# Optimization experiments

Hardware: AMD Instinct MI355X
Metric: run time of the kernel (lower is better)

## Reference

```python
import jax, jax.numpy as jnp
import numpy as np

D_MIN, D_MAX, D_COUNT = 2.0, 22.0, 36  # RFdiffusion rbf() constants


def _rbf(D):
    # D: [..., L, L] -> [..., L, L, D_COUNT]
    mu = jnp.linspace(D_MIN, D_MAX, D_COUNT, dtype=D.dtype)
    sigma = (D_MAX - D_MIN) / D_COUNT
    return jnp.exp(-(((D[..., None] - mu) / sigma) ** 2))


def _layernorm(x, w, b, eps=1e-5):
    mu = jnp.mean(x, axis=-1, keepdims=True)
    var = jnp.var(x, axis=-1, keepdims=True)
    return (x - mu) * jax.lax.rsqrt(var + eps) * w + b


def setup_inputs() -> dict:
    key = jax.random.key(0)
    ks = jax.random.split(key, 8)
    B, L, d_state, d_pair, h, d_rbf = 1, 512, 256, 128, 32, D_COUNT
    s = lambda d: 1.0 / np.sqrt(d)
    return {
        "xyz": jax.random.normal(ks[0], (B, L, 3, 3), jnp.float32) * 5.0,
        "state": jax.random.normal(ks[1], (B, L, d_state), jnp.float32),
        "ln_w": jnp.ones((d_state,), jnp.float32),
        "ln_b": jnp.zeros((d_state,), jnp.float32),
        "w_rbf": jax.random.normal(ks[2], (d_rbf, d_pair), jnp.float32) * s(d_rbf),
        "b_rbf": jnp.zeros((d_pair,), jnp.float32),
        "w_left": jax.random.normal(ks[3], (d_state, h), jnp.float32) * s(d_state),
        "b_left": jnp.zeros((h,), jnp.float32),
        "w_right": jax.random.normal(ks[4], (d_state, h), jnp.float32) * s(d_state),
        "b_right": jnp.zeros((h,), jnp.float32),
        "w_gate": jax.random.normal(ks[5], (h * h, d_pair), jnp.float32) * s(h * h),
        "b_gate": jnp.zeros((d_pair,), jnp.float32),
    }


def reference(xyz, state, ln_w, ln_b, w_rbf, b_rbf, w_left, b_left,
              w_right, b_right, w_gate, b_gate):
    B, L = xyz.shape[:2]
    h = w_left.shape[1]
    d_pair = w_rbf.shape[1]

    # pairwise CA distances -> RBF features -> project to pair dim
    cas = xyz[:, :, 1]                                        # [B, L, 3]
    d2 = jnp.sum((cas[:, :, None, :] - cas[:, None, :, :]) ** 2, axis=-1)
    dist = jnp.sqrt(jnp.maximum(d2, 1e-12))                   # [B, L, L]
    rbf_feat = _rbf(dist) @ w_rbf + b_rbf                     # [B, L, L, d_pair]

    # gated pair bias: sigmoid(to_gate(outer(left, right)))
    st = _layernorm(state, ln_w, ln_b)
    left = st @ w_left + b_left                               # [B, L, h]
    right = st @ w_right + b_right                            # [B, L, h]

    # Algebraically identical to einsum('bli,bmj->blmij') -> reshape -> Linear,
    # but factored through the projection weight to avoid the O(L^2 h^2) tensor.
    Wg = w_gate.reshape(h, h, d_pair)                         # flatten order i*h+j
    t = jnp.einsum('bli,ijp->bljp', left, Wg)                 # [B, L, h, d_pair]
    logits = jnp.einsum('bljp,bmj->blmp', t, right) + b_gate  # [B, L, L, d_pair]
    gate = jax.nn.sigmoid(logits)

    return gate * rbf_feat
```

## Files before the change

kernel.cpp:

```cpp
#include <hip/hip_runtime.h>
#include <hip/hip_fp16.h>

typedef _Float16 half8 __attribute__((ext_vector_type(8)));
typedef float floatx4 __attribute__((ext_vector_type(4)));

#define LSEQ 512
#define DSTATE 256
#define DPAIR 128
#define HH 32
#define DRBF 36

#define MUSTEP (20.0f / 35.0f)
#define INVSIG 1.8f

__global__ __launch_bounds__(256) void prologA(
    const float* __restrict__ state, const float* __restrict__ ln_w,
    const float* __restrict__ ln_b, const float* __restrict__ w_left,
    const float* __restrict__ b_left, const float* __restrict__ w_right,
    const float* __restrict__ b_right, float* __restrict__ left,
    _Float16* __restrict__ right_h) {
  __shared__ float stS[DSTATE];
  __shared__ float redS[4], redQ[4];
  __shared__ float part[4][64];
  const int l = blockIdx.x, tid = threadIdx.x;

  float x = state[l * DSTATE + tid];
  float s = x, q = x * x;
  #pragma unroll
  for (int o = 32; o > 0; o >>= 1) {
    s += __shfl_down(s, o);
    q += __shfl_down(q, o);
  }
  if ((tid & 63) == 0) { redS[tid >> 6] = s; redQ[tid >> 6] = q; }
  __syncthreads();
  float tot = redS[0] + redS[1] + redS[2] + redS[3];
  float totq = redQ[0] + redQ[1] + redQ[2] + redQ[3];
  float mean = tot * (1.0f / DSTATE);
  float var = totq * (1.0f / DSTATE) - mean * mean;
  float inv = rsqrtf(var + 1e-5f);
  stS[tid] = (x - mean) * inv * ln_w[tid] + ln_b[tid];
  __syncthreads();

  const int j = tid & 63;
  const int quarter = tid >> 6;
  const float* __restrict__ w = (j < HH) ? (w_left + j) : (w_right + (j - HH));
  const int c0 = quarter * 64;
  float acc = 0.0f;
  #pragma unroll 8
  for (int cc = 0; cc < 64; ++cc) acc += stS[c0 + cc] * w[(c0 + cc) * HH];
  part[quarter][j] = acc;
  __syncthreads();
  if (tid < 64) {
    float sum = part[0][tid] + part[1][tid] + part[2][tid] + part[3][tid];
    if (tid < HH)
      left[l * HH + tid] = sum + b_left[tid];
    else
      right_h[l * HH + (tid - HH)] = (_Float16)(sum + b_right[tid - HH]);
  }
}

__global__ __launch_bounds__(256) void prologB(
    const float* __restrict__ w_gate, const float* __restrict__ w_rbf,
    const float* __restrict__ left, _Float16* __restrict__ tT,
    _Float16* __restrict__ w_rbfT) {
  const int tid = threadIdx.x;
  if (blockIdx.x == 1024) {
    for (int e = tid; e < DPAIR * 64; e += 256) {
      int p = e >> 6, k = e & 63;
      w_rbfT[e] = (k < DRBF) ? (_Float16)w_rbf[k * DPAIR + p] : (_Float16)0.0f;
    }
    return;
  }
  const int c = blockIdx.x & 15;
  const int lc = blockIdx.x >> 4;
  const int j = tid & 31;
  const int p = c * 8 + (tid >> 5);

  float wcol[32];
  #pragma unroll
  for (int i = 0; i < 32; ++i) wcol[i] = w_gate[(i * HH + j) * DPAIR + p];

  const int l0 = lc * 8;
  #pragma unroll
  for (int l = l0; l < l0 + 8; ++l) {
    const float* __restrict__ lf = left + l * HH;
    float acc = 0.0f;
    #pragma unroll
    for (int i = 0; i < 32; ++i) acc += lf[i] * wcol[i];
    tT[l * (DPAIR * HH) + c * 256 + tid] = (_Float16)acc;
  }
}

__global__ __launch_bounds__(256) void mainC(
    const float* __restrict__ xyz, const float* __restrict__ b_rbf,
    const float* __restrict__ b_gate, const _Float16* __restrict__ right_h,
    const _Float16* __restrict__ tT, const _Float16* __restrict__ w_rbfT,
    float* __restrict__ out) {
  __shared__ _Float16 sT[DPAIR * HH];
  __shared__ _Float16 sW[DPAIR * 64];
  const int l = blockIdx.x >> 1;
  const int half = blockIdx.x & 1;
  const int tid = threadIdx.x;
  const int wave = tid >> 6;
  const int lane = tid & 63;
  const int ln16 = lane & 15;
  const int quad = lane >> 4;

  {
    const uint4* __restrict__ src = (const uint4*)(tT + (size_t)l * (DPAIR * HH));
    uint4* dst = (uint4*)sT;
    #pragma unroll
    for (int i = 0; i < 2; ++i) dst[tid + 256 * i] = src[tid + 256 * i];
    const uint4* __restrict__ src2 = (const uint4*)w_rbfT;
    uint4* dst2 = (uint4*)sW;
    #pragma unroll
    for (int i = 0; i < 4; ++i) dst2[tid + 256 * i] = src2[tid + 256 * i];
  }

  const float clx = xyz[l * 9 + 3];
  const float cly = xyz[l * 9 + 4];
  const float clz = xyz[l * 9 + 5];

  float bg[8], br[8];
  #pragma unroll
  for (int pt = 0; pt < 8; ++pt) {
    bg[pt] = b_gate[pt * 16 + ln16];
    br[pt] = b_rbf[pt * 16 + ln16];
  }

  __syncthreads();

  const int mt0 = half * 16;
  for (int mt = mt0 + wave; mt < mt0 + 16; mt += 4) {
    const int mA = mt * 16 + ln16;
    half8 Ar = *(const half8*)(right_h + mA * HH + quad * 8);

    const float dx = clx - xyz[mA * 9 + 3];
    const float dy = cly - xyz[mA * 9 + 4];
    const float dz = clz - xyz[mA * 9 + 5];
    const float d = sqrtf(fmaxf(dx * dx + dy * dy + dz * dz, 1e-12f));

    half8 A0, A1;
    #pragma unroll
    for (int jj = 0; jj < 8; ++jj) {
      const int k = quad * 8 + jj;
      const float u = (d - (2.0f + (float)k * MUSTEP)) * INVSIG;
      A0[jj] = (_Float16)__expf(-u * u);
    }
    #pragma unroll
    for (int jj = 0; jj < 8; ++jj) {
      const int k = 32 + quad * 8 + jj;
      float v = 0.0f;
      if (k < DRBF) {
        const float u = (d - (2.0f + (float)k * MUSTEP)) * INVSIG;
        v = __expf(-u * u);
      }
      A1[jj] = (_Float16)v;
    }

    #pragma unroll
    for (int pt = 0; pt < 8; ++pt) {
      const int p = pt * 16 + ln16;
      half8 Bt = *(const half8*)(sT + p * HH + quad * 8);
      half8 Bw0 = *(const half8*)(sW + p * 64 + quad * 8);
      half8 Bw1 = *(const half8*)(sW + p * 64 + 32 + quad * 8);

      floatx4 accL = {0.f, 0.f, 0.f, 0.f};
      floatx4 accR = {0.f, 0.f, 0.f, 0.f};
      accL = __builtin_amdgcn_mfma_f32_16x16x32_f16(Ar, Bt, accL, 0, 0, 0);
      accR = __builtin_amdgcn_mfma_f32_16x16x32_f16(A0, Bw0, accR, 0, 0, 0);
      accR = __builtin_amdgcn_mfma_f32_16x16x32_f16(A1, Bw1, accR, 0, 0, 0);

      float* orow = out + ((size_t)l * LSEQ + mt * 16 + quad * 4) * DPAIR + p;
      #pragma unroll
      for (int i = 0; i < 4; ++i) {
        const float logit = accL[i] + bg[pt];
        const float gate = __builtin_amdgcn_rcpf(1.0f + __expf(-logit));
        const float feat = accR[i] + br[pt];
        orow[i * DPAIR] = gate * feat;
      }
    }
  }
}

extern "C" void kernel_launch(void* const* d_in, const int* in_sizes, int n_in,
                              void* d_out, int out_size, void* d_ws,
                              size_t ws_size, hipStream_t stream) {
  const float* xyz = (const float*)d_in[0];
  const float* state = (const float*)d_in[1];
  const float* ln_w = (const float*)d_in[2];
  const float* ln_b = (const float*)d_in[3];
  const float* w_rbf = (const float*)d_in[4];
  const float* b_rbf = (const float*)d_in[5];
  const float* w_left = (const float*)d_in[6];
  const float* b_left = (const float*)d_in[7];
  const float* w_right = (const float*)d_in[8];
  const float* b_right = (const float*)d_in[9];
  const float* w_gate = (const float*)d_in[10];
  const float* b_gate = (const float*)d_in[11];
  float* out = (float*)d_out;

  char* ws = (char*)d_ws;
  float* left = (float*)ws;
  _Float16* right_h = (_Float16*)(ws + 65536);
  _Float16* tT = (_Float16*)(ws + 98304);
  _Float16* w_rbfT = (_Float16*)(ws + 4292608);

  prologA<<<512, 256, 0, stream>>>(state, ln_w, ln_b, w_left, b_left, w_right,
                                   b_right, left, right_h);
  prologB<<<1025, 256, 0, stream>>>(w_gate, w_rbf, left, tT, w_rbfT);
  mainC<<<1024, 256, 0, stream>>>(xyz, b_rbf, b_gate, right_h, tT, w_rbfT, out);
}
```

Before: 190.2 us.

## Fuse layernorm/projection and gate-weight contraction into one prolog kernel

```diff
diff --git a/kernel.cpp b/kernel.cpp
--- a/kernel.cpp
+++ b/kernel.cpp
@@ -13,81 +13,124 @@
 #define MUSTEP (20.0f / 35.0f)
 #define INVSIG 1.8f
 
-__global__ __launch_bounds__(256) void prologA(
+__global__ __launch_bounds__(256) void prolog(
     const float* __restrict__ state, const float* __restrict__ ln_w,
     const float* __restrict__ ln_b, const float* __restrict__ w_left,
     const float* __restrict__ b_left, const float* __restrict__ w_right,
-    const float* __restrict__ b_right, float* __restrict__ left,
-    _Float16* __restrict__ right_h) {
-  __shared__ float stS[DSTATE];
-  __shared__ float redS[4], redQ[4];
-  __shared__ float part[4][64];
-  const int l = blockIdx.x, tid = threadIdx.x;
-
-  float x = state[l * DSTATE + tid];
-  float s = x, q = x * x;
-  #pragma unroll
-  for (int o = 32; o > 0; o >>= 1) {
-    s += __shfl_down(s, o);
-    q += __shfl_down(q, o);
-  }
-  if ((tid & 63) == 0) { redS[tid >> 6] = s; redQ[tid >> 6] = q; }
-  __syncthreads();
-  float tot = redS[0] + redS[1] + redS[2] + redS[3];
-  float totq = redQ[0] + redQ[1] + redQ[2] + redQ[3];
-  float mean = tot * (1.0f / DSTATE);
-  float var = totq * (1.0f / DSTATE) - mean * mean;
-  float inv = rsqrtf(var + 1e-5f);
-  stS[tid] = (x - mean) * inv * ln_w[tid] + ln_b[tid];
-  __syncthreads();
-
-  const int j = tid & 63;
-  const int quarter = tid >> 6;
-  const float* __restrict__ w = (j < HH) ? (w_left + j) : (w_right + (j - HH));
-  const int c0 = quarter * 64;
-  float acc = 0.0f;
-  #pragma unroll 8
-  for (int cc = 0; cc < 64; ++cc) acc += stS[c0 + cc] * w[(c0 + cc) * HH];
-  part[quarter][j] = acc;
-  __syncthreads();
-  if (tid < 64) {
-    float sum = part[0][tid] + part[1][tid] + part[2][tid] + part[3][tid];
-    if (tid < HH)
-      left[l * HH + tid] = sum + b_left[tid];
-    else
-      right_h[l * HH + (tid - HH)] = (_Float16)(sum + b_right[tid - HH]);
-  }
-}
-
-__global__ __launch_bounds__(256) void prologB(
-    const float* __restrict__ w_gate, const float* __restrict__ w_rbf,
-    const float* __restrict__ left, _Float16* __restrict__ tT,
-    _Float16* __restrict__ w_rbfT) {
+    const float* __restrict__ b_right, const float* __restrict__ w_gate,
+    const float* __restrict__ w_rbf, _Float16* __restrict__ right_h,
+    _Float16* __restrict__ tT, _Float16* __restrict__ w_rbfT) {
   const int tid = threadIdx.x;
-  if (blockIdx.x == 1024) {
+  if (blockIdx.x == 256) {
     for (int e = tid; e < DPAIR * 64; e += 256) {
       int p = e >> 6, k = e & 63;
       w_rbfT[e] = (k < DRBF) ? (_Float16)w_rbf[k * DPAIR + p] : (_Float16)0.0f;
     }
     return;
   }
-  const int c = blockIdx.x & 15;
-  const int lc = blockIdx.x >> 4;
-  const int j = tid & 31;
-  const int p = c * 8 + (tid >> 5);
-
-  float wcol[32];
+  const int l0 = blockIdx.x * 2;
+
+  __shared__ float stS[2][DSTATE];
+  __shared__ float redS[2][4], redQ[2][4];
+  __shared__ float part[2][4][64];
+  __shared__ float sL[2][HH];
+  __shared__ _Float16 sTT[2][DPAIR * HH];
+
+  float x0 = state[l0 * DSTATE + tid];
+  float x1 = state[(l0 + 1) * DSTATE + tid];
+  float s0 = x0, q0 = x0 * x0, s1 = x1, q1 = x1 * x1;
   #pragma unroll
-  for (int i = 0; i < 32; ++i) wcol[i] = w_gate[(i * HH + j) * DPAIR + p];
-
-  const int l0 = lc * 8;
-  #pragma unroll
-  for (int l = l0; l < l0 + 8; ++l) {
-    const float* __restrict__ lf = left + l * HH;
-    float acc = 0.0f;
-    #pragma unroll
-    for (int i = 0; i < 32; ++i) acc += lf[i] * wcol[i];
-    tT[l * (DPAIR * HH) + c * 256 + tid] = (_Float16)acc;
+  for (int o = 32; o > 0; o >>= 1) {
+    s0 += __shfl_down(s0, o);
+    q0 += __shfl_down(q0, o);
+    s1 += __shfl_down(s1, o);
+    q1 += __shfl_down(q1, o);
+  }
+  if ((tid & 63) == 0) {
+    redS[0][tid >> 6] = s0; redQ[0][tid >> 6] = q0;
+    redS[1][tid >> 6] = s1; redQ[1][tid >> 6] = q1;
+  }
+  __syncthreads();
+  {
+    const float lw = ln_w[tid], lb = ln_b[tid];
+    float tot0 = redS[0][0] + redS[0][1] + redS[0][2] + redS[0][3];
+    float totq0 = redQ[0][0] + redQ[0][1] + redQ[0][2] + redQ[0][3];
+    float tot1 = redS[1][0] + redS[1][1] + redS[1][2] + redS[1][3];
+    float totq1 = redQ[1][0] + redQ[1][1] + redQ[1][2] + redQ[1][3];
+    float m0 = tot0 * (1.0f / DSTATE);
+    float m1 = tot1 * (1.0f / DSTATE);
+    float inv0 = rsqrtf(totq0 * (1.0f / DSTATE) - m0 * m0 + 1e-5f);
+    float inv1 = rsqrtf(totq1 * (1.0f / DSTATE) - m1 * m1 + 1e-5f);
+    stS[0][tid] = (x0 - m0) * inv0 * lw + lb;
+    stS[1][tid] = (x1 - m1) * inv1 * lw + lb;
+  }
+  __syncthreads();
+
+  {
+    const int j = tid & 63, quarter = tid >> 6, c0 = quarter * 64;
+    const float* __restrict__ w =
+        (j < HH) ? (w_left + j) : (w_right + (j - HH));
+    float a0 = 0.0f, a1 = 0.0f;
+    #pragma unroll 8
+    for (int cc = 0; cc < 64; ++cc) {
+      const float wv = w[(c0 + cc) * HH];
+      a0 += stS[0][c0 + cc] * wv;
+      a1 += stS[1][c0 + cc] * wv;
+    }
+    part[0][quarter][j] = a0;
+    part[1][quarter][j] = a1;
+  }
+  __syncthreads();
+  if (tid < 128) {
+    const int r = tid >> 6, jj = tid & 63;
+    float sum = part[r][0][jj] + part[r][1][jj] + part[r][2][jj] + part[r][3][jj];
+    if (jj < HH)
+      sL[r][jj] = sum + b_left[jj];
+    else
+      right_h[(l0 + r) * HH + (jj - HH)] = (_Float16)(sum + b_right[jj - HH]);
+  }
+  __syncthreads();
+
+  {
+    const int j3 = tid >> 3;
+    const int pc = tid & 7;
+    float acc0[16], acc1[16];
+    #pragma unroll
+    for (int k = 0; k < 16; ++k) { acc0[k] = 0.0f; acc1[k] = 0.0f; }
+    #pragma unroll 4
+    for (int i = 0; i < 32; ++i) {
+      const float la0 = sL[0][i], la1 = sL[1][i];
+      const float4* __restrict__ wrow =
+          (const float4*)(w_gate + (i * HH + j3) * DPAIR + pc * 16);
+      float wv[16];
+      *(float4*)(wv + 0) = wrow[0];
+      *(float4*)(wv + 4) = wrow[1];
+      *(float4*)(wv + 8) = wrow[2];
+      *(float4*)(wv + 12) = wrow[3];
+      #pragma unroll
+      for (int k = 0; k < 16; ++k) {
+        acc0[k] += la0 * wv[k];
+        acc1[k] += la1 * wv[k];
+      }
+    }
+    #pragma unroll
+    for (int k = 0; k < 16; ++k) {
+      const int p = pc * 16 + k;
+      sTT[0][p * HH + j3] = (_Float16)acc0[k];
+      sTT[1][p * HH + j3] = (_Float16)acc1[k];
+    }
+  }
+  __syncthreads();
+
+  {
+    const uint4* __restrict__ s0p = (const uint4*)sTT[0];
+    const uint4* __restrict__ s1p = (const uint4*)sTT[1];
+    uint4* g0 = (uint4*)(tT + (size_t)l0 * (DPAIR * HH));
+    uint4* g1 = (uint4*)(tT + (size_t)(l0 + 1) * (DPAIR * HH));
+    g0[tid] = s0p[tid];
+    g0[tid + 256] = s0p[tid + 256];
+    g1[tid] = s1p[tid];
+    g1[tid + 256] = s1p[tid + 256];
   }
 }
 
@@ -130,6 +173,14 @@
 
   __syncthreads();
 
+  half8 Bw0[8], Bw1[8];
+  #pragma unroll
+  for (int pt = 0; pt < 8; ++pt) {
+    const int p = pt * 16 + ln16;
+    Bw0[pt] = *(const half8*)(sW + p * 64 + quad * 8);
+    Bw1[pt] = *(const half8*)(sW + p * 64 + 32 + quad * 8);
+  }
+
   const int mt0 = half * 16;
   for (int mt = mt0 + wave; mt < mt0 + 16; mt += 4) {
     const int mA = mt * 16 + ln16;
@@ -162,14 +213,12 @@
     for (int pt = 0; pt < 8; ++pt) {
       const int p = pt * 16 + ln16;
       half8 Bt = *(const half8*)(sT + p * HH + quad * 8);
-      half8 Bw0 = *(const half8*)(sW + p * 64 + quad * 8);
-      half8 Bw1 = *(const half8*)(sW + p * 64 + 32 + quad * 8);
 
       floatx4 accL = {0.f, 0.f, 0.f, 0.f};
       floatx4 accR = {0.f, 0.f, 0.f, 0.f};
       accL = __builtin_amdgcn_mfma_f32_16x16x32_f16(Ar, Bt, accL, 0, 0, 0);
-      accR = __builtin_amdgcn_mfma_f32_16x16x32_f16(A0, Bw0, accR, 0, 0, 0);
-      accR = __builtin_amdgcn_mfma_f32_16x16x32_f16(A1, Bw1, accR, 0, 0, 0);
+      accR = __builtin_amdgcn_mfma_f32_16x16x32_f16(A0, Bw0[pt], accR, 0, 0, 0);
+      accR = __builtin_amdgcn_mfma_f32_16x16x32_f16(A1, Bw1[pt], accR, 0, 0, 0);
 
       float* orow = out + ((size_t)l * LSEQ + mt * 16 + quad * 4) * DPAIR + p;
       #pragma unroll
@@ -201,13 +250,11 @@
   float* out = (float*)d_out;
 
   char* ws = (char*)d_ws;
-  float* left = (float*)ws;
-  _Float16* right_h = (_Float16*)(ws + 65536);
-  _Float16* tT = (_Float16*)(ws + 98304);
-  _Float16* w_rbfT = (_Float16*)(ws + 4292608);
-
-  prologA<<<512, 256, 0, stream>>>(state, ln_w, ln_b, w_left, b_left, w_right,
-                                   b_right, left, right_h);
-  prologB<<<1025, 256, 0, stream>>>(w_gate, w_rbf, left, tT, w_rbfT);
+  _Float16* right_h = (_Float16*)ws;
+  _Float16* tT = (_Float16*)(ws + 32768);
+  _Float16* w_rbfT = (_Float16*)(ws + 32768 + 4194304);
+
+  prolog<<<257, 256, 0, stream>>>(state, ln_w, ln_b, w_left, b_left, w_right,
+                                  b_right, w_gate, w_rbf, right_h, tT, w_rbfT);
   mainC<<<1024, 256, 0, stream>>>(xyz, b_rbf, b_gate, right_h, tT, w_rbfT, out);
 }
```

Result: no change. 189.7 us (-0.3%).
